# Kernel tuning notes

Measured on AMD Instinct MI355X. Metric: run time of the kernel, lower is better.

## Reference

```python
import jax, jax.numpy as jnp
import numpy as np

V, D, L, H, F, S = 32000, 1024, 6, 16, 4096, 1024
B, T = 2, 1024
DH = D // H
EPS = 1e-5


def layer_norm(x, w, b):
    m = jnp.mean(x, axis=-1, keepdims=True)
    v = jnp.var(x, axis=-1, keepdims=True)
    return (x - m) * jax.lax.rsqrt(v + EPS) * w + b


def setup_inputs() -> dict:
    key = jax.random.key(0)
    ks = jax.random.split(key, 12)
    n = lambda k, shape: jax.random.normal(k, shape, jnp.float32) * 0.02
    return {
        "idx": jax.random.randint(ks[0], (B, T), 0, V),
        "tok_emb": n(ks[1], (V, D)),
        "pos_emb": n(ks[2], (S, D)),
        "ln1_w": jnp.ones((L, D), jnp.float32),
        "ln1_b": jnp.zeros((L, D), jnp.float32),
        "wq": n(ks[3], (L, D, D)),
        "wk": n(ks[4], (L, D, D)),
        "wv": n(ks[5], (L, D, D)),
        "proj": n(ks[6], (L, D, D)),
        "ln2_w": jnp.ones((L, D), jnp.float32),
        "ln2_b": jnp.zeros((L, D), jnp.float32),
        "fc1_w": n(ks[7], (L, F, D)),
        "fc1_b": jnp.zeros((L, F), jnp.float32),
        "fc2_w": n(ks[8], (L, D, F)),
        "fc2_b": jnp.zeros((L, D), jnp.float32),
        "lnf_w": jnp.ones((D,), jnp.float32),
        "lnf_b": jnp.zeros((D,), jnp.float32),
        "head_w": n(ks[9], (V, D)),
    }


def reference(idx, tok_emb, pos_emb, ln1_w, ln1_b, wq, wk, wv, proj,
              ln2_w, ln2_b, fc1_w, fc1_b, fc2_w, fc2_b, lnf_w, lnf_b, head_w):
    b, t = idx.shape
    x = tok_emb[idx] + pos_emb[:t][None, :, :]  # [B,T,D]
    causal = jnp.tril(jnp.ones((t, t), bool))

    def block(x, p):
        l1w, l1b, Wq, Wk, Wv, Wp, l2w, l2b, F1w, F1b, F2w, F2b = p
        h = layer_norm(x, l1w, l1b)
        q = (h @ Wq.T).reshape(b, t, H, DH).transpose(0, 2, 1, 3)  # [B,H,T,dh]
        k = (h @ Wk.T).reshape(b, t, H, DH).transpose(0, 2, 1, 3)
        v = (h @ Wv.T).reshape(b, t, H, DH).transpose(0, 2, 1, 3)
        # muP attention: 1/d_head scaling (not 1/sqrt(d_head))
        att = jnp.einsum('bhqd,bhkd->bhqk', q, k) * (1.0 / DH)
        att = jnp.where(causal, att, -jnp.inf)
        att = jax.nn.softmax(att, axis=-1)
        y = jnp.einsum('bhqk,bhkd->bhqd', att, v)
        y = y.transpose(0, 2, 1, 3).reshape(b, t, D)
        x = x + y @ Wp.T
        h = layer_norm(x, l2w, l2b)
        h = jax.nn.gelu(h @ F1w.T + F1b, approximate=False)  # torch F.gelu = exact erf
        x = x + (h @ F2w.T + F2b)
        return x, None

    x, _ = jax.lax.scan(block, x, (ln1_w, ln1_b, wq, wk, wv, proj,
                                   ln2_w, ln2_b, fc1_w, fc1_b, fc2_w, fc2_b))
    x = layer_norm(x, lnf_w, lnf_b)
    return x @ head_w.T  # [B,T,V] logits (MuReadout with unit multipliers)
```

## Files before the change

kernel.cpp:

```cpp
#include <hip/hip_runtime.h>
#include <cmath>

typedef __bf16 bf16_t;
typedef bf16_t bf16x8 __attribute__((ext_vector_type(8)));
typedef bf16_t bf16x4 __attribute__((ext_vector_type(4)));
typedef float floatx4 __attribute__((ext_vector_type(4)));

#define B_ 2
#define T_ 1024
#define D_ 1024
#define H_ 16
#define DH_ 64
#define L_ 6
#define F_ 4096
#define V_ 32000
#define NTOK (B_ * T_)

__global__ __launch_bounds__(256) void detect_kernel(
    const unsigned short* __restrict__ tok, int* __restrict__ flag)
{
  __shared__ int cnt;
  if (threadIdx.x == 0) cnt = 0;
  __syncthreads();
  int c = 0;
#pragma unroll
  for (int i = 0; i < 16; i++) {
    unsigned short h = tok[threadIdx.x * 16 + i];
    int e = (h >> 7) & 0xFF;
    if (e >= 134) c++;
  }
  atomicAdd(&cnt, c);
  __syncthreads();
  if (threadIdx.x == 0) *flag = (cnt > 64) ? 1 : 0;
}

__device__ inline bf16x8 load8(const void* p, size_t i, int fp32m) {
  bf16x8 r;
  if (fp32m) {
    const float* f = (const float*)p + i;
    float4 v0 = *(const float4*)f;
    float4 v1 = *(const float4*)(f + 4);
    r[0] = (bf16_t)v0.x; r[1] = (bf16_t)v0.y; r[2] = (bf16_t)v0.z; r[3] = (bf16_t)v0.w;
    r[4] = (bf16_t)v1.x; r[5] = (bf16_t)v1.y; r[6] = (bf16_t)v1.z; r[7] = (bf16_t)v1.w;
  } else {
    r = *(const bf16x8*)((const bf16_t*)p + i);
  }
  return r;
}

__device__ inline float loadf(const void* p, size_t i, int fp32m) {
  return fp32m ? ((const float*)p)[i] : (float)((const bf16_t*)p)[i];
}

__global__ __launch_bounds__(256) void convflat_kernel(
    const void* __restrict__ src, bf16_t* __restrict__ dst,
    const int* __restrict__ modep, long n)
{
  int fp32m = *modep;
  size_t i = ((size_t)blockIdx.x * 256 + threadIdx.x) * 8;
  if ((long)i >= n) return;
  bf16x8 r = load8(src, i, fp32m);
  *(bf16x8*)(dst + i) = r;
}

__global__ __launch_bounds__(256) void convqkv_kernel(
    const void* __restrict__ wq, const void* __restrict__ wk,
    const void* __restrict__ wv, bf16_t* __restrict__ dst,
    const int* __restrict__ modep)
{
  int fp32m = *modep;
  size_t i = ((size_t)blockIdx.x * 256 + threadIdx.x) * 8;
  const size_t per = (size_t)D_ * D_;
  int lm = (int)(i / per);
  size_t off = i - (size_t)lm * per;
  int l = lm / 3, mat = lm - l * 3;
  const void* src = (mat == 0) ? wq : ((mat == 1) ? wk : wv);
  bf16x8 r = load8(src, (size_t)l * per + off, fp32m);
  *(bf16x8*)(dst + i) = r;
}

__global__ __launch_bounds__(256) void embed_kernel(
    const int* __restrict__ idx, const void* __restrict__ tok,
    const void* __restrict__ pos, float* __restrict__ x,
    const int* __restrict__ modep)
{
  int fp32m = *modep;
  int row = blockIdx.x;
  int t = row & (T_ - 1);
  int tokid = idx[row];
  int c = threadIdx.x * 4;
  float tv[4], pv[4];
  if (fp32m) {
    float4 a = *(const float4*)((const float*)tok + (size_t)tokid * D_ + c);
    float4 b = *(const float4*)((const float*)pos + (size_t)t * D_ + c);
    tv[0] = a.x; tv[1] = a.y; tv[2] = a.z; tv[3] = a.w;
    pv[0] = b.x; pv[1] = b.y; pv[2] = b.z; pv[3] = b.w;
  } else {
    bf16x4 a = *(const bf16x4*)((const bf16_t*)tok + (size_t)tokid * D_ + c);
    bf16x4 b = *(const bf16x4*)((const bf16_t*)pos + (size_t)t * D_ + c);
#pragma unroll
    for (int j = 0; j < 4; j++) { tv[j] = (float)a[j]; pv[j] = (float)b[j]; }
  }
  float4 o;
  o.x = tv[0] + pv[0]; o.y = tv[1] + pv[1];
  o.z = tv[2] + pv[2]; o.w = tv[3] + pv[3];
  *(float4*)(x + (size_t)row * D_ + c) = o;
}

__global__ __launch_bounds__(256) void ln_kernel(
    const float* __restrict__ x, const void* __restrict__ w,
    const void* __restrict__ bb, bf16_t* __restrict__ out,
    const int* __restrict__ modep, int woff)
{
  int fp32m = *modep;
  int row = blockIdx.x, tid = threadIdx.x;
  int lane = tid & 63, wid = tid >> 6;
  const float* xr = x + (size_t)row * D_;
  float4 xv = ((const float4*)xr)[tid];
  float s = xv.x + xv.y + xv.z + xv.w;
  float sq = xv.x * xv.x + xv.y * xv.y + xv.z * xv.z + xv.w * xv.w;
#pragma unroll
  for (int off = 32; off; off >>= 1) {
    s += __shfl_xor(s, off);
    sq += __shfl_xor(sq, off);
  }
  __shared__ float ss[4], ssq[4];
  if (lane == 0) { ss[wid] = s; ssq[wid] = sq; }
  __syncthreads();
  s = ss[0] + ss[1] + ss[2] + ss[3];
  sq = ssq[0] + ssq[1] + ssq[2] + ssq[3];
  float mean = s * (1.f / D_);
  float var = sq * (1.f / D_) - mean * mean;
  var = fmaxf(var, 0.f);
  float rstd = rsqrtf(var + 1e-5f);
  int c = tid * 4;
  float xa[4] = {xv.x, xv.y, xv.z, xv.w};
  bf16x4 ov;
#pragma unroll
  for (int j = 0; j < 4; j++) {
    float wj = loadf(w, (size_t)woff + c + j, fp32m);
    float bj = loadf(bb, (size_t)woff + c + j, fp32m);
    ov[j] = (bf16_t)((xa[j] - mean) * rstd * wj + bj);
  }
  *(bf16x4*)(out + (size_t)row * D_ + c) = ov;
}

__device__ inline float gelu_f(float v) {
  return 0.5f * v * (1.f + erff(v * 0.70710678118654752f));
}

__device__ inline void gload16(void* lds, const void* g) {
  __builtin_amdgcn_global_load_lds(
      (__attribute__((address_space(1))) void*)(g),
      (__attribute__((address_space(3))) void*)(lds), 16, 0, 0);
}

template<int BM, int BN>
__global__ __launch_bounds__(256) void gemm_t(
    const bf16_t* __restrict__ A, const bf16_t* __restrict__ W,
    const void* __restrict__ bias, size_t boff, const float* __restrict__ res,
    bf16_t* __restrict__ outb, float* __restrict__ outf, void* __restrict__ outx,
    const int* __restrict__ modep, int M, int N, int K, int dogelu, int mshift)
{
  constexpr int MT = BM / 32, NT = BN / 32;
  __shared__ __align__(16) bf16_t As[BM * 32];
  __shared__ __align__(16) bf16_t Bs[BN * 32];
  int fp32m = *modep;
  int tid = threadIdx.x;
  int lane = tid & 63, wid = tid >> 6;
  int wm = wid & 1, wn = wid >> 1;
  int nwg = gridDim.x, bid = blockIdx.x;
  int qq = nwg >> 3, rr = nwg & 7;
  int xcd = bid & 7, ii = bid >> 3;
  int wg = (xcd < rr ? xcd * (qq + 1) : rr * (qq + 1) + (xcd - rr) * qq) + ii;
  int m0 = (wg & ((1 << mshift) - 1)) * BM;
  int n0 = (wg >> mshift) * BN;
  int ln15 = lane & 15, q4 = lane >> 4;
  int srow = tid >> 2, scol = (tid & 3) * 8;
  const bf16_t* Ag[BM / 64];
  const bf16_t* Wg[BN / 64];
#pragma unroll
  for (int hh = 0; hh < BM / 64; hh++)
    Ag[hh] = A + (size_t)(m0 + hh * 64 + srow) * K + scol;
#pragma unroll
  for (int hh = 0; hh < BN / 64; hh++)
    Wg[hh] = W + (size_t)(n0 + hh * 64 + srow) * K + scol;
  floatx4 acc[MT][NT] = {};
  for (int k0 = 0; k0 < K; k0 += 32) {
    __syncthreads();
#pragma unroll
    for (int hh = 0; hh < BM / 64; hh++)
      gload16(&As[hh * 2048 + tid * 8], Ag[hh] + k0);
#pragma unroll
    for (int hh = 0; hh < BN / 64; hh++)
      gload16(&Bs[hh * 2048 + tid * 8], Wg[hh] + k0);
    __syncthreads();
    bf16x8 a[MT], b[NT];
#pragma unroll
    for (int i = 0; i < MT; i++)
      a[i] = *(const bf16x8*)&As[(wm * (BM / 2) + i * 16 + ln15) * 32 + q4 * 8];
#pragma unroll
    for (int j = 0; j < NT; j++)
      b[j] = *(const bf16x8*)&Bs[(wn * (BN / 2) + j * 16 + ln15) * 32 + q4 * 8];
#pragma unroll
    for (int mt = 0; mt < MT; mt++)
#pragma unroll
      for (int nt = 0; nt < NT; nt++)
        acc[mt][nt] = __builtin_amdgcn_mfma_f32_16x16x32_bf16(a[mt], b[nt], acc[mt][nt], 0, 0, 0);
  }
#pragma unroll
  for (int mt = 0; mt < MT; mt++)
#pragma unroll
    for (int nt = 0; nt < NT; nt++) {
      int col = n0 + wn * (BN / 2) + nt * 16 + ln15;
      float bv = bias ? loadf(bias, boff + col, fp32m) : 0.f;
#pragma unroll
      for (int r = 0; r < 4; r++) {
        int row = m0 + wm * (BM / 2) + mt * 16 + q4 * 4 + r;
        float v = acc[mt][nt][r] + bv;
        if (dogelu) v = gelu_f(v);
        size_t o = (size_t)row * N + col;
        if (res) v += res[o];
        if (outf) outf[o] = v;
        if (outb) outb[o] = (bf16_t)v;
        if (outx) {
          if (fp32m) ((float*)outx)[o] = v;
          else ((bf16_t*)outx)[o] = (bf16_t)v;
        }
      }
    }
}

__global__ __launch_bounds__(256) void gemm_bt(
    const bf16_t* __restrict__ A, const void* __restrict__ W, size_t woffs,
    const void* __restrict__ bias, size_t boff, const float* __restrict__ res,
    bf16_t* __restrict__ outb, float* __restrict__ outf, void* __restrict__ outx,
    const int* __restrict__ modep, int M, int N, int K, int dogelu)
{
  __shared__ __align__(16) bf16_t As[64][40];
  __shared__ __align__(16) bf16_t Bs[64][40];
  int fp32m = *modep;
  int tid = threadIdx.x;
  int lane = tid & 63, wid = tid >> 6;
  int wm = wid & 1, wn = wid >> 1;
  int m0 = blockIdx.y * 64, n0 = blockIdx.x * 64;
  int srow = tid >> 2, scol = (tid & 3) * 8;
  const bf16_t* Ap = A + (size_t)(m0 + srow) * K + scol;
  size_t wrow = woffs + (size_t)(n0 + srow) * K + scol;
  floatx4 acc[2][2] = {};
  int ln15 = lane & 15, q4 = lane >> 4;
  for (int k0 = 0; k0 < K; k0 += 32) {
    __syncthreads();
    *(bf16x8*)&As[srow][scol] = *(const bf16x8*)(Ap + k0);
    *(bf16x8*)&Bs[srow][scol] = load8(W, wrow + k0, fp32m);
    __syncthreads();
    bf16x8 a0 = *(const bf16x8*)&As[wm * 32 + ln15][q4 * 8];
    bf16x8 a1 = *(const bf16x8*)&As[wm * 32 + 16 + ln15][q4 * 8];
    bf16x8 b0 = *(const bf16x8*)&Bs[wn * 32 + ln15][q4 * 8];
    bf16x8 b1 = *(const bf16x8*)&Bs[wn * 32 + 16 + ln15][q4 * 8];
    acc[0][0] = __builtin_amdgcn_mfma_f32_16x16x32_bf16(a0, b0, acc[0][0], 0, 0, 0);
    acc[0][1] = __builtin_amdgcn_mfma_f32_16x16x32_bf16(a0, b1, acc[0][1], 0, 0, 0);
    acc[1][0] = __builtin_amdgcn_mfma_f32_16x16x32_bf16(a1, b0, acc[1][0], 0, 0, 0);
    acc[1][1] = __builtin_amdgcn_mfma_f32_16x16x32_bf16(a1, b1, acc[1][1], 0, 0, 0);
  }
#pragma unroll
  for (int mt = 0; mt < 2; mt++)
#pragma unroll
    for (int nt = 0; nt < 2; nt++) {
      int col = n0 + wn * 32 + nt * 16 + ln15;
      float bv = bias ? loadf(bias, boff + col, fp32m) : 0.f;
#pragma unroll
      for (int r = 0; r < 4; r++) {
        int row = m0 + wm * 32 + mt * 16 + q4 * 4 + r;
        float v = acc[mt][nt][r] + bv;
        if (dogelu) v = gelu_f(v);
        size_t o = (size_t)row * N + col;
        if (res) v += res[o];
        if (outf) outf[o] = v;
        if (outb) outb[o] = (bf16_t)v;
        if (outx) {
          if (fp32m) ((float*)outx)[o] = v;
          else ((bf16_t*)outx)[o] = (bf16_t)v;
        }
      }
    }
}

__global__ __launch_bounds__(256) void attn_mfma(
    const bf16_t* __restrict__ qkv, bf16_t* __restrict__ y)
{
  __shared__ __align__(16) bf16_t Ks[64][72];
  __shared__ __align__(16) bf16_t Vt[64][72];
  __shared__ __align__(16) bf16_t Ps[4][16][72];
  int tid = threadIdx.x;
  int lane = tid & 63, w = tid >> 6;
  int ln15 = lane & 15, g = lane >> 4;
  int idxb = blockIdx.x;
  int phase = idxb >> 8, slot = idxb & 255;
  int bh = slot >> 3, jj = slot & 7;
  int qb = phase ? jj : (15 - jj);
  int b = bh >> 4, h = bh & 15;
  int q0 = qb * 64;
  int qrow = q0 + w * 16;
  const bf16_t* kp = qkv + 1024;
  const bf16_t* vp = qkv + 2048;
  bf16x8 qa0, qa1;
  {
    size_t base = ((size_t)(b * T_ + qrow + ln15)) * 3072 + h * 64 + g * 8;
    qa0 = *(const bf16x8*)(qkv + base);
    qa1 = *(const bf16x8*)(qkv + base + 32);
  }
  floatx4 o[4] = {};
  float m_i[4], l_i[4];
#pragma unroll
  for (int r = 0; r < 4; r++) { m_i[r] = -__builtin_inff(); l_i[r] = 0.f; }
  int ntile = qb + 1;
  int sr = tid >> 2, sc = (tid & 3) * 16;
  for (int it = 0; it < ntile; it++) {
    int k0 = it * 64;
    __syncthreads();
    size_t gb = ((size_t)(b * T_ + k0 + sr)) * 3072 + h * 64 + sc;
    bf16x8 kv0 = *(const bf16x8*)(kp + gb);
    bf16x8 kv1 = *(const bf16x8*)(kp + gb + 8);
    bf16x8 vv0 = *(const bf16x8*)(vp + gb);
    bf16x8 vv1 = *(const bf16x8*)(vp + gb + 8);
    *(bf16x8*)&Ks[sr][sc] = kv0;
    *(bf16x8*)&Ks[sr][sc + 8] = kv1;
#pragma unroll
    for (int e = 0; e < 8; e++) {
      int d0 = sc + e, d1 = sc + 8 + e;
      Vt[d0][sr ^ (((d0 >> 3) & 7) << 3)] = vv0[e];
      Vt[d1][sr ^ (((d1 >> 3) & 7) << 3)] = vv1[e];
    }
    __syncthreads();
    floatx4 s[4] = {};
#pragma unroll
    for (int nt = 0; nt < 4; nt++) {
      bf16x8 b0 = *(const bf16x8*)&Ks[nt * 16 + ln15][g * 8];
      bf16x8 b1 = *(const bf16x8*)&Ks[nt * 16 + ln15][32 + g * 8];
      s[nt] = __builtin_amdgcn_mfma_f32_16x16x32_bf16(qa0, b0, s[nt], 0, 0, 0);
      s[nt] = __builtin_amdgcn_mfma_f32_16x16x32_bf16(qa1, b1, s[nt], 0, 0, 0);
    }
    int last = (it == ntile - 1);
    float p[4][4];
    float mt[4];
#pragma unroll
    for (int r = 0; r < 4; r++) mt[r] = -__builtin_inff();
#pragma unroll
    for (int nt = 0; nt < 4; nt++)
#pragma unroll
      for (int r = 0; r < 4; r++) {
        float sv = s[nt][r] * 0.015625f;
        if (last && (k0 + nt * 16 + ln15) > (qrow + g * 4 + r))
          sv = -__builtin_inff();
        p[nt][r] = sv;
        mt[r] = fmaxf(mt[r], sv);
      }
#pragma unroll
    for (int off = 1; off < 16; off <<= 1)
#pragma unroll
      for (int r = 0; r < 4; r++) mt[r] = fmaxf(mt[r], __shfl_xor(mt[r], off));
    float alpha[4];
#pragma unroll
    for (int r = 0; r < 4; r++) {
      float mn = fmaxf(m_i[r], mt[r]);
      alpha[r] = __expf(m_i[r] - mn);
      m_i[r] = mn;
    }
    float rs[4] = {0.f, 0.f, 0.f, 0.f};
#pragma unroll
    for (int nt = 0; nt < 4; nt++)
#pragma unroll
      for (int r = 0; r < 4; r++) {
        float pv = __expf(p[nt][r] - m_i[r]);
        rs[r] += pv;
        Ps[w][g * 4 + r][nt * 16 + ln15] = (bf16_t)pv;
      }
#pragma unroll
    for (int off = 1; off < 16; off <<= 1)
#pragma unroll
      for (int r = 0; r < 4; r++) rs[r] += __shfl_xor(rs[r], off);
#pragma unroll
    for (int r = 0; r < 4; r++) l_i[r] = l_i[r] * alpha[r] + rs[r];
#pragma unroll
    for (int nt = 0; nt < 4; nt++)
#pragma unroll
      for (int r = 0; r < 4; r++) o[nt][r] *= alpha[r];
#pragma unroll
    for (int ks = 0; ks < 2; ks++) {
      bf16x8 pa = *(const bf16x8*)&Ps[w][ln15][ks * 32 + g * 8];
#pragma unroll
      for (int nt = 0; nt < 4; nt++) {
        int d = nt * 16 + ln15;
        bf16x8 vb = *(const bf16x8*)&Vt[d][(ks * 32 + g * 8) ^ (((d >> 3) & 7) << 3)];
        o[nt] = __builtin_amdgcn_mfma_f32_16x16x32_bf16(pa, vb, o[nt], 0, 0, 0);
      }
    }
  }
#pragma unroll
  for (int nt = 0; nt < 4; nt++)
#pragma unroll
    for (int r = 0; r < 4; r++) {
      size_t orow = (size_t)(b * T_ + qrow + g * 4 + r) * D_ + h * 64 + nt * 16 + ln15;
      y[orow] = (bf16_t)(o[nt][r] / l_i[r]);
    }
}

__global__ __launch_bounds__(256) void attn_kernel(
    const bf16_t* __restrict__ q, const bf16_t* __restrict__ k,
    const bf16_t* __restrict__ v, bf16_t* __restrict__ y, int stride)
{
  __shared__ float Kt[64][65];
  __shared__ float Vt[64][65];
  __shared__ float qs[4][64];
  __shared__ float ps[4][64];
  int tid = threadIdx.x;
  int lane = tid & 63, w = tid >> 6;
  int blk = blockIdx.x;
  int tqblk = blk & 255;
  int bh = blk >> 8;
  int b = bh >> 4, hh = bh & 15;
  int tq_base = tqblk * 4;
  int tq = tq_base + w;
  size_t qrow = ((size_t)(b * T_ + tq)) * stride + hh * DH_;
  qs[w][lane] = (float)q[qrow + lane];
  float m_i = -INFINITY, l_i = 0.f, acc = 0.f;
  int ntiles = (tq_base >> 6) + 1;
  int lr = tid >> 2, lc = (tid & 3) * 16;
  for (int it = 0; it < ntiles; it++) {
    int tk0 = it * 64;
    __syncthreads();
    size_t gbase = ((size_t)(b * T_ + tk0 + lr)) * stride + hh * DH_ + lc;
    bf16x8 kv0 = *(const bf16x8*)(k + gbase);
    bf16x8 kv1 = *(const bf16x8*)(k + gbase + 8);
    bf16x8 vv0 = *(const bf16x8*)(v + gbase);
    bf16x8 vv1 = *(const bf16x8*)(v + gbase + 8);
#pragma unroll
    for (int j = 0; j < 8; j++) {
      Kt[lr][lc + j] = (float)kv0[j];
      Kt[lr][lc + 8 + j] = (float)kv1[j];
      Vt[lr][lc + j] = (float)vv0[j];
      Vt[lr][lc + 8 + j] = (float)vv1[j];
    }
    __syncthreads();
    int tk = tk0 + lane;
    float s = -INFINITY;
    if (tk <= tq) {
      float a = 0.f;
#pragma unroll
      for (int d = 0; d < 64; d++) a += qs[w][d] * Kt[lane][d];
      s = a * (1.f / 64.f);
    }
    float mt = s;
#pragma unroll
    for (int off = 32; off; off >>= 1) mt = fmaxf(mt, __shfl_xor(mt, off));
    float mnew = fmaxf(m_i, mt);
    float alpha = (m_i == -INFINITY) ? 0.f : expf(m_i - mnew);
    float p = (tk <= tq) ? expf(s - mnew) : 0.f;
    float psum = p;
#pragma unroll
    for (int off = 32; off; off >>= 1) psum += __shfl_xor(psum, off);
    l_i = l_i * alpha + psum;
    ps[w][lane] = p;
    float pv = 0.f;
#pragma unroll
    for (int j = 0; j < 64; j++) pv += ps[w][j] * Vt[j][lane];
    acc = acc * alpha + pv;
    m_i = mnew;
  }
  y[((size_t)(b * T_ + tq)) * D_ + hh * DH_ + lane] = (bf16_t)(acc / l_i);
}

template<int BM, int BN>
static inline void launch_gemm_t(const bf16_t* A, const bf16_t* W,
                                 const void* bias, size_t boff, const float* res,
                                 bf16_t* outb, float* outf, void* outx,
                                 const int* modep, int M, int N, int K,
                                 int dogelu, hipStream_t s)
{
  int nMB = M / BM;
  int mshift = (nMB == 16) ? 4 : ((nMB == 32) ? 5 : 31 - __builtin_clz(nMB));
  int nwg = nMB * (N / BN);
  gemm_t<BM, BN><<<dim3(nwg), dim3(256), 0, s>>>(
      A, W, bias, boff, res, outb, outf, outx, modep, M, N, K, dogelu, mshift);
}

static inline void launch_gemm_old(const bf16_t* A, const void* W, size_t woffs,
                                   const void* bias, size_t boff, const float* res,
                                   bf16_t* outb, float* outf, void* outx,
                                   const int* modep, int M, int N, int K,
                                   int dogelu, hipStream_t s)
{
  dim3 g(N / 64, M / 64);
  gemm_bt<<<g, dim3(256), 0, s>>>(A, W, woffs, bias, boff, res, outb, outf,
                                  outx, modep, M, N, K, dogelu);
}

#define OFF_X      256ull
#define OFF_H      8388864ull
#define OFF_QKV    12583168ull
#define OFF_Y      25166080ull
#define OFF_HF     29360384ull
#define OFF_WQKV   46137600ull
#define OFF_WPROJ  83886336ull
#define OFF_WFC1   96469248ull
#define OFF_WFC2   146800896ull
#define OFF_WHEAD  197132544ull
#define REQ_WS     262668544ull

extern "C" void kernel_launch(void* const* d_in, const int* in_sizes, int n_in,
                              void* d_out, int out_size, void* d_ws, size_t ws_size,
                              hipStream_t stream)
{
  (void)in_sizes; (void)n_in; (void)out_size;
  const int* idx      = (const int*)d_in[0];
  const void* tok_emb = d_in[1];
  const void* pos_emb = d_in[2];
  const void* ln1_w   = d_in[3];
  const void* ln1_b   = d_in[4];
  const void* wq      = d_in[5];
  const void* wk      = d_in[6];
  const void* wv      = d_in[7];
  const void* wproj   = d_in[8];
  const void* ln2_w   = d_in[9];
  const void* ln2_b   = d_in[10];
  const void* fc1_w   = d_in[11];
  const void* fc1_b   = d_in[12];
  const void* fc2_w   = d_in[13];
  const void* fc2_b   = d_in[14];
  const void* lnf_w   = d_in[15];
  const void* lnf_b   = d_in[16];
  const void* head_w  = d_in[17];

  char* ws = (char*)d_ws;
  int* modep = (int*)ws;
  detect_kernel<<<1, 256, 0, stream>>>((const unsigned short*)tok_emb, modep);

  if (ws_size >= REQ_WS) {
    float*  x   = (float*)(ws + OFF_X);
    bf16_t* h   = (bf16_t*)(ws + OFF_H);
    bf16_t* qkv = (bf16_t*)(ws + OFF_QKV);
    bf16_t* yb  = (bf16_t*)(ws + OFF_Y);
    bf16_t* hf  = (bf16_t*)(ws + OFF_HF);
    bf16_t* wqkvb = (bf16_t*)(ws + OFF_WQKV);
    bf16_t* wprjb = (bf16_t*)(ws + OFF_WPROJ);
    bf16_t* wfc1b = (bf16_t*)(ws + OFF_WFC1);
    bf16_t* wfc2b = (bf16_t*)(ws + OFF_WFC2);
    bf16_t* whedb = (bf16_t*)(ws + OFF_WHEAD);

    convqkv_kernel<<<9216, 256, 0, stream>>>(wq, wk, wv, wqkvb, modep);
    convflat_kernel<<<3072, 256, 0, stream>>>(wproj, wprjb, modep, (long)L_ * D_ * D_);
    convflat_kernel<<<12288, 256, 0, stream>>>(fc1_w, wfc1b, modep, (long)L_ * F_ * D_);
    convflat_kernel<<<12288, 256, 0, stream>>>(fc2_w, wfc2b, modep, (long)L_ * D_ * F_);
    convflat_kernel<<<16000, 256, 0, stream>>>(head_w, whedb, modep, (long)V_ * D_);

    embed_kernel<<<NTOK, 256, 0, stream>>>(idx, tok_emb, pos_emb, x, modep);

    for (int l = 0; l < L_; l++) {
      size_t wd = (size_t)l * D_ * D_;
      size_t wf = (size_t)l * F_ * D_;
      ln_kernel<<<NTOK, 256, 0, stream>>>(x, ln1_w, ln1_b, h, modep, l * D_);
      launch_gemm_t<64, 128>(h, wqkvb + (size_t)l * 3 * D_ * D_, nullptr, 0,
                             nullptr, qkv, nullptr, nullptr, modep,
                             NTOK, 3 * D_, D_, 0, stream);
      attn_mfma<<<512, 256, 0, stream>>>(qkv, yb);
      launch_gemm_t<64, 64>(yb, wprjb + wd, nullptr, 0, x, nullptr, x, nullptr,
                            modep, NTOK, D_, D_, 0, stream);
      ln_kernel<<<NTOK, 256, 0, stream>>>(x, ln2_w, ln2_b, h, modep, l * D_);
      launch_gemm_t<128, 128>(h, wfc1b + wf, fc1_b, (size_t)l * F_, nullptr, hf,
                              nullptr, nullptr, modep, NTOK, F_, D_, 1, stream);
      launch_gemm_t<64, 64>(hf, wfc2b + wf, fc2_b, (size_t)l * D_, x, nullptr, x,
                            nullptr, modep, NTOK, D_, F_, 0, stream);
    }

    ln_kernel<<<NTOK, 256, 0, stream>>>(x, lnf_w, lnf_b, h, modep, 0);
    launch_gemm_t<128, 128>(h, whedb, nullptr, 0, nullptr, nullptr, nullptr,
                            d_out, modep, NTOK, V_, D_, 0, stream);
  } else {
    float*  x  = (float*)(ws + 256);
    bf16_t* h  = (bf16_t*)(ws + 8388864);
    bf16_t* qb = (bf16_t*)(ws + 12583168);
    bf16_t* kb = (bf16_t*)(ws + 16777472);
    bf16_t* vb = (bf16_t*)(ws + 20971776);
    bf16_t* yb = (bf16_t*)(ws + 25166080);
    bf16_t* hf = (bf16_t*)(ws + 29360384);

    embed_kernel<<<NTOK, 256, 0, stream>>>(idx, tok_emb, pos_emb, x, modep);

    for (int l = 0; l < L_; l++) {
      size_t wd = (size_t)l * D_ * D_;
      size_t wf = (size_t)l * F_ * D_;
      ln_kernel<<<NTOK, 256, 0, stream>>>(x, ln1_w, ln1_b, h, modep, l * D_);
      launch_gemm_old(h, wq, wd, nullptr, 0, nullptr, qb, nullptr, nullptr,
                      modep, NTOK, D_, D_, 0, stream);
      launch_gemm_old(h, wk, wd, nullptr, 0, nullptr, kb, nullptr, nullptr,
                      modep, NTOK, D_, D_, 0, stream);
      launch_gemm_old(h, wv, wd, nullptr, 0, nullptr, vb, nullptr, nullptr,
                      modep, NTOK, D_, D_, 0, stream);
      attn_kernel<<<B_ * H_ * (T_ / 4), 256, 0, stream>>>(qb, kb, vb, yb, D_);
      launch_gemm_old(yb, wproj, wd, nullptr, 0, x, nullptr, x, nullptr,
                      modep, NTOK, D_, D_, 0, stream);
      ln_kernel<<<NTOK, 256, 0, stream>>>(x, ln2_w, ln2_b, h, modep, l * D_);
      launch_gemm_old(h, fc1_w, wf, fc1_b, (size_t)l * F_, nullptr, hf, nullptr,
                      nullptr, modep, NTOK, F_, D_, 1, stream);
      launch_gemm_old(hf, fc2_w, wf, fc2_b, (size_t)l * D_, x, nullptr, x,
                      nullptr, modep, NTOK, D_, F_, 0, stream);
    }

    ln_kernel<<<NTOK, 256, 0, stream>>>(x, lnf_w, lnf_b, h, modep, 0);
    launch_gemm_old(h, head_w, 0, nullptr, 0, nullptr, nullptr, nullptr, d_out,
                    modep, NTOK, V_, D_, 0, stream);
  }
}
```

Baseline: 2.319 ms.

## Double-buffer GEMM LDS tiles with async prefetch two tiles ahead

```diff
diff --git a/kernel.cpp b/kernel.cpp
--- a/kernel.cpp
+++ b/kernel.cpp
@@ -163,8 +163,9 @@
     const int* __restrict__ modep, int M, int N, int K, int dogelu, int mshift)
 {
   constexpr int MT = BM / 32, NT = BN / 32;
-  __shared__ __align__(16) bf16_t As[BM * 32];
-  __shared__ __align__(16) bf16_t Bs[BN * 32];
+  constexpr int NL = BM / 64 + BN / 64;
+  __shared__ __align__(16) bf16_t As[2][BM * 32];
+  __shared__ __align__(16) bf16_t Bs[2][BN * 32];
   int fp32m = *modep;
   int tid = threadIdx.x;
   int lane = tid & 63, wid = tid >> 6;
@@ -185,28 +186,46 @@
 #pragma unroll
   for (int hh = 0; hh < BN / 64; hh++)
     Wg[hh] = W + (size_t)(n0 + hh * 64 + srow) * K + scol;
+
+  auto stage = [&](int t, int buf) {
+    int k0 = t * 32;
+#pragma unroll
+    for (int hh = 0; hh < BM / 64; hh++)
+      gload16(&As[buf][hh * 2048 + tid * 8], Ag[hh] + k0);
+#pragma unroll
+    for (int hh = 0; hh < BN / 64; hh++)
+      gload16(&Bs[buf][hh * 2048 + tid * 8], Wg[hh] + k0);
+  };
+
+  int ktiles = K / 32;
+  stage(0, 0);
+  if (ktiles > 1) stage(1, 1);
   floatx4 acc[MT][NT] = {};
-  for (int k0 = 0; k0 < K; k0 += 32) {
-    __syncthreads();
-#pragma unroll
-    for (int hh = 0; hh < BM / 64; hh++)
-      gload16(&As[hh * 2048 + tid * 8], Ag[hh] + k0);
-#pragma unroll
-    for (int hh = 0; hh < BN / 64; hh++)
-      gload16(&Bs[hh * 2048 + tid * 8], Wg[hh] + k0);
-    __syncthreads();
+  for (int t = 0; t < ktiles; ++t) {
+    int cur = t & 1;
+    if (t + 1 < ktiles)
+      asm volatile("s_waitcnt vmcnt(%0)" :: "i"(NL) : "memory");
+    else
+      asm volatile("s_waitcnt vmcnt(0)" ::: "memory");
+    __builtin_amdgcn_s_barrier();
+    asm volatile("" ::: "memory");
     bf16x8 a[MT], b[NT];
 #pragma unroll
     for (int i = 0; i < MT; i++)
-      a[i] = *(const bf16x8*)&As[(wm * (BM / 2) + i * 16 + ln15) * 32 + q4 * 8];
+      a[i] = *(const bf16x8*)&As[cur][(wm * (BM / 2) + i * 16 + ln15) * 32 + q4 * 8];
 #pragma unroll
     for (int j = 0; j < NT; j++)
-      b[j] = *(const bf16x8*)&Bs[(wn * (BN / 2) + j * 16 + ln15) * 32 + q4 * 8];
+      b[j] = *(const bf16x8*)&Bs[cur][(wn * (BN / 2) + j * 16 + ln15) * 32 + q4 * 8];
+    __builtin_amdgcn_s_setprio(1);
 #pragma unroll
     for (int mt = 0; mt < MT; mt++)
 #pragma unroll
       for (int nt = 0; nt < NT; nt++)
         acc[mt][nt] = __builtin_amdgcn_mfma_f32_16x16x32_bf16(a[mt], b[nt], acc[mt][nt], 0, 0, 0);
+    __builtin_amdgcn_s_setprio(0);
+    asm volatile("" ::: "memory");
+    __builtin_amdgcn_s_barrier();
+    if (t + 2 < ktiles) stage(t + 2, cur);
   }
 #pragma unroll
   for (int mt = 0; mt < MT; mt++)
```

Result: faster. 2.187 ms (-5.7%).
